# Performance work log

Hardware: AMD Instinct MI355X
Metric: run time of the kernel (lower is better)

## Reference

```python
import jax, jax.numpy as jnp
import numpy as np

N, E, F, T = 10000, 160000, 4, 12   # nodes, edges, features, periods
C, HID, OUT = 512, 256, 12          # tgcn out_channels, head hidden, output_dim


def setup_inputs() -> dict:
    key = jax.random.key(0)
    ks = jax.random.split(key, 24)
    g = lambda k, s: (jax.random.normal(k, s, dtype=jnp.float32) * 0.05)
    inp = {
        "x": jax.random.normal(ks[0], (N, F, T), dtype=jnp.float32),
        "edge_index": jax.random.randint(ks[1], (2, E), 0, N, dtype=jnp.int32),
        "edge_attr": jax.random.uniform(ks[2], (E,), dtype=jnp.float32),
        "att": g(ks[3], (T,)),
        # TGCN gates: GCNConv (W [F,C], b [C]) + Linear on cat([conv, H]) ([2C,C], [C])
        "Wz_g": g(ks[4], (F, C)), "bz_g": jnp.zeros((C,), jnp.float32),
        "Wz_l": g(ks[5], (2 * C, C)), "bz_l": jnp.zeros((C,), jnp.float32),
        "Wr_g": g(ks[6], (F, C)), "br_g": jnp.zeros((C,), jnp.float32),
        "Wr_l": g(ks[7], (2 * C, C)), "br_l": jnp.zeros((C,), jnp.float32),
        "Wh_g": g(ks[8], (F, C)), "bh_g": jnp.zeros((C,), jnp.float32),
        "Wh_l": g(ks[9], (2 * C, C)), "bh_l": jnp.zeros((C,), jnp.float32),
        # dense head
        "W1": g(ks[10], (C, HID)), "b1": jnp.zeros((HID,), jnp.float32),
        "W2": g(ks[11], (HID, OUT)), "b2": jnp.zeros((OUT,), jnp.float32),
    }
    return inp


def reference(x, edge_index, edge_attr, att,
              Wz_g, bz_g, Wz_l, bz_l,
              Wr_g, br_g, Wr_l, br_l,
              Wh_g, bh_g, Wh_l, bh_l,
              W1, b1, W2, b2):
    n = x.shape[0]
    # GCN normalization with self loops (fill value 1.0), computed once
    loops = jnp.arange(n, dtype=edge_index.dtype)
    src = jnp.concatenate([edge_index[0], loops])
    dst = jnp.concatenate([edge_index[1], loops])
    w = jnp.concatenate([edge_attr, jnp.ones((n,), x.dtype)])
    deg = jax.ops.segment_sum(w, dst, num_segments=n)
    dinv = jax.lax.rsqrt(jnp.maximum(deg, 1e-12))
    norm = dinv[src] * w * dinv[dst]  # [E+N]

    def gcn(xt, W, b):
        xw = xt @ W                                   # [N,C]
        msg = norm[:, None] * xw[src]                 # gather over edges
        return jax.ops.segment_sum(msg, dst, num_segments=n) + b

    probs = jax.nn.softmax(att)            # attention over periods
    xt_seq = jnp.moveaxis(x, -1, 0)        # [T,N,F]
    H0 = jnp.zeros((n, C), x.dtype)

    def step(carry, inp):
        H, acc = carry
        xt, p = inp
        z = jax.nn.sigmoid(jnp.concatenate([gcn(xt, Wz_g, bz_g), H], axis=1) @ Wz_l + bz_l)
        r = jax.nn.sigmoid(jnp.concatenate([gcn(xt, Wr_g, br_g), H], axis=1) @ Wr_l + br_l)
        ht = jnp.tanh(jnp.concatenate([gcn(xt, Wh_g, bh_g), H * r], axis=1) @ Wh_l + bh_l)
        Hn = z * H + (1.0 - z) * ht
        return (Hn, acc + p * Hn), None

    (Hf, H_accum), _ = jax.lax.scan(step, (H0, H0), (xt_seq, probs))
    out_hidden = H_accum
    h = jax.nn.relu(H_accum)
    h = jax.nn.relu(h @ W1 + b1)
    h = h @ W2 + b2
    return (h, out_hidden)
```

## Files before the change

### kernel.cpp

```cpp
#include <hip/hip_runtime.h>
#include <math.h>

#define NF 48
#define TT 12

typedef __bf16 v8bf __attribute__((ext_vector_type(8)));
typedef float v16f __attribute__((ext_vector_type(16)));

__device__ __forceinline__ void gld16(const void* g, void* l) {
  __builtin_amdgcn_global_load_lds(
      (const __attribute__((address_space(1))) void*)(uintptr_t)g,
      (__attribute__((address_space(3))) void*)(uintptr_t)l, 16, 0, 0);
}


__global__ void k_init(float* __restrict__ deg, int* __restrict__ cnt, int n) {
  int i = blockIdx.x * blockDim.x + threadIdx.x;
  if (i < n) { deg[i] = 1.0f; cnt[i] = 0; cnt[n + i] = 0; }
}

__global__ void k_edge(const int* __restrict__ dst, const float* __restrict__ w,
                       float* __restrict__ deg, int* __restrict__ cnt, int e) {
  int i = blockIdx.x * blockDim.x + threadIdx.x;
  if (i < e) {
    int d = dst[i];
    atomicAdd(&deg[d], w[i]);
    atomicAdd(&cnt[d], 1);
  }
}


__global__ void k_scan1(const int* __restrict__ cnt, int* __restrict__ pscan,
                        int* __restrict__ bsum, const float* __restrict__ deg,
                        float* __restrict__ dinv, int n) {
  __shared__ int s[256];
  int i = blockIdx.x * 256 + threadIdx.x;
  int v = (i < n) ? cnt[i] : 0;
  s[threadIdx.x] = v;
  __syncthreads();
  for (int off = 1; off < 256; off <<= 1) {
    int t = 0;
    if (threadIdx.x >= off) t = s[threadIdx.x - off];
    __syncthreads();
    s[threadIdx.x] += t;
    __syncthreads();
  }
  if (i < n) {
    pscan[i] = s[threadIdx.x] - v;
    dinv[i] = rsqrtf(fmaxf(deg[i], 1e-12f));
  }
  if (threadIdx.x == 255) bsum[blockIdx.x] = s[255];
}

__global__ void k_scan2(const int* __restrict__ bsum, int* __restrict__ bpre, int nb,
                        const float* __restrict__ att, float* __restrict__ probs) {
  if (blockIdx.x == 0 && threadIdx.x == 0) {
    int run = 0;
    for (int b = 0; b < nb; b++) { bpre[b] = run; run += bsum[b]; }
  }
  if (blockIdx.x == 0 && threadIdx.x == 64) {
    float m = -1e30f;
    for (int t = 0; t < TT; t++) m = fmaxf(m, att[t]);
    float e[TT], s = 0.f;
    for (int t = 0; t < TT; t++) { e[t] = expf(att[t] - m); s += e[t]; }
    for (int t = 0; t < TT; t++) probs[t] = e[t] / s;
  }
}

__global__ void k_scan3(const int* __restrict__ pscan, const int* __restrict__ bpre,
                        int* __restrict__ offs, int n, int e) {
  int i = blockIdx.x * blockDim.x + threadIdx.x;
  if (i < n) offs[i] = pscan[i] + bpre[i >> 8];
  if (i == 0) offs[n] = e;
}

__global__ void k_place(const int* __restrict__ src, const int* __restrict__ dst,
                        const float* __restrict__ w, const int* __restrict__ offs,
                        int* __restrict__ fill, int* __restrict__ csrc,
                        float* __restrict__ cw, int e) {
  int i = blockIdx.x * blockDim.x + threadIdx.x;
  if (i >= e) return;
  int d = dst[i];
  int p = offs[d] + atomicAdd(&fill[d], 1);
  csrc[p] = src[i];
  cw[p] = w[i];
}

__global__ void k_gather(const int* __restrict__ offs, const int* __restrict__ csrc,
                         const float* __restrict__ cw, const float* __restrict__ dinv,
                         const float* __restrict__ x, float* __restrict__ Y, int n) {
  int tg = blockIdx.x * blockDim.x + threadIdx.x;
  if (tg >= n * 12) return;
  int i = tg / 12, q = tg % 12;
  float di = dinv[i];
  const float4* x4 = (const float4*)x;
  float4 sv = x4[(size_t)i * 12 + q];
  float ax = di * sv.x, ay = di * sv.y, az = di * sv.z, aw = di * sv.w;
  int e1 = offs[i + 1];
  for (int e = offs[i]; e < e1; e++) {
    int s = csrc[e];
    float wv = cw[e] * dinv[s];
    float4 xv = x4[(size_t)s * 12 + q];
    ax = fmaf(wv, xv.x, ax); ay = fmaf(wv, xv.y, ay);
    az = fmaf(wv, xv.z, az); aw = fmaf(wv, xv.w, aw);
  }
  float4 o = make_float4(di * ax, di * ay, di * az, di * aw);
  ((float4*)Y)[(size_t)i * 12 + q] = o;
}

__device__ __forceinline__ size_t packIdx128(int n, int k) {
  int row = n & 127;
  int c = (k & 31) >> 3;
  return (size_t)(n >> 7) * (128 * 512) + (size_t)(k >> 5) * (128 * 32) +
         (size_t)row * 32 + (size_t)((c ^ (row & 3)) << 3) + (k & 7);
}

__global__ void k_pack3(const float* __restrict__ Wzl, const float* __restrict__ Wrl,
                        const float* __restrict__ Whl, const float* __restrict__ W1,
                        __bf16* __restrict__ WzrP, __bf16* __restrict__ WhP,
                        __bf16* __restrict__ W1P) {
  __shared__ __bf16 t[64][72];
  int modew = blockIdx.z;
  if (modew == 1 && blockIdx.x >= 8) return;
  if (modew == 2 && blockIdx.x >= 4) return;
  int n0 = blockIdx.x * 64, k0 = blockIdx.y * 64;
  __bf16* WT = (modew == 0) ? WzrP : (modew == 1) ? WhP : W1P;
#pragma unroll
  for (int p = 0; p < 4; p++) {
    int kk = p * 16 + (threadIdx.x >> 4);
    int nn = (threadIdx.x & 15) * 4;
    int n = n0 + nn, k = k0 + kk;
    float4 v;
    if (modew == 2) {
      v = *(const float4*)(W1 + (size_t)k * 256 + n);
    } else {
      const float* src = (modew == 1) ? Whl : Wzl;
      int nc = n;
      if (modew == 0 && n >= 512) { src = Wrl; nc = n - 512; }
      v = *(const float4*)(src + (size_t)(512 + k) * 512 + nc);
    }
    t[kk][nn + 0] = (__bf16)v.x; t[kk][nn + 1] = (__bf16)v.y;
    t[kk][nn + 2] = (__bf16)v.z; t[kk][nn + 3] = (__bf16)v.w;
  }
  __syncthreads();
#pragma unroll
  for (int u = 0; u < 2; u++) {
    int unit = threadIdx.x * 2 + u;
    int nl = unit >> 3, kg = unit & 7;
    v8bf o;
#pragma unroll
    for (int j = 0; j < 8; j++) o[j] = t[kg * 8 + j][nl];
    *(v8bf*)(WT + packIdx128(n0 + nl, k0 + kg * 8)) = o;
  }
}

__global__ void k_build_eff3(const float* __restrict__ Wzg, const float* __restrict__ Wzl,
                             const float* __restrict__ bzg, const float* __restrict__ bzl,
                             const float* __restrict__ Wrg, const float* __restrict__ Wrl,
                             const float* __restrict__ brg, const float* __restrict__ brl,
                             const float* __restrict__ Whg, const float* __restrict__ Whl,
                             const float* __restrict__ bhg, const float* __restrict__ bhl,
                             float* __restrict__ WzrE, float* __restrict__ bzrE,
                             float* __restrict__ WhE, float* __restrict__ bhE) {
  int idx = blockIdx.x * blockDim.x + threadIdx.x;
  if (idx >= 3 * 5 * 512) return;
  int seg = idx / 2560;
  int r = (idx % 2560) / 512, c = idx % 512;
  const float *Wg, *Wl, *bg, *bl;
  float *We, *be;
  int ostride, ooff;
  if (seg == 0) { Wg = Wzg; Wl = Wzl; bg = bzg; bl = bzl; We = WzrE; be = bzrE; ostride = 1024; ooff = 0; }
  else if (seg == 1) { Wg = Wrg; Wl = Wrl; bg = brg; bl = brl; We = WzrE; be = bzrE; ostride = 1024; ooff = 512; }
  else { Wg = Whg; Wl = Whl; bg = bhg; bl = bhl; We = WhE; be = bhE; ostride = 512; ooff = 0; }
  float s = 0.f;
  if (r < 4) {
    for (int k = 0; k < 512; k++) s += Wg[r * 512 + k] * Wl[k * 512 + c];
    We[r * ostride + ooff + c] = s;
  } else {
    for (int k = 0; k < 512; k++) s += bg[k] * Wl[k * 512 + c];
    be[ooff + c] = s + bl[c];
  }
}

__global__ void k_wy3(const float* __restrict__ WzrE, const float* __restrict__ bzrE,
                      const float* __restrict__ WhE, const float* __restrict__ bhE,
                      const float* __restrict__ b1,
                      __bf16* __restrict__ WyZR, __bf16* __restrict__ WyH,
                      __bf16* __restrict__ Wy1) {
  int idx = blockIdx.x * blockDim.x + threadIdx.x;
  const float* Weff; const float* beff; __bf16* out; int Nout, loc;
  if (idx < 1024 * 16) { Weff = WzrE; beff = bzrE; out = WyZR; Nout = 1024; loc = idx; }
  else if (idx < (1024 + 512) * 16) { Weff = WhE; beff = bhE; out = WyH; Nout = 512; loc = idx - 1024 * 16; }
  else if (idx < (1024 + 512 + 256) * 16) { Weff = nullptr; beff = b1; out = Wy1; Nout = 256; loc = idx - (1024 + 512) * 16; }
  else return;
  int n = loc >> 4, k = loc & 15;
  float v = 0.f;
  if (k < 4) v = Weff ? Weff[k * Nout + n] : 0.f;
  else if (k == 4) v = beff[n];
  out[(size_t)(n >> 7) * 2048 + (size_t)(n & 127) * 16 + k] = (__bf16)v;
}

__global__ void k_yat0(const float* __restrict__ Y,
                       const float* __restrict__ WzrE, const float* __restrict__ bzrE,
                       const float* __restrict__ WhE, const float* __restrict__ bhE,
                       __bf16* __restrict__ Ya, __bf16* __restrict__ H1, int n) {
  int idx = blockIdx.x * blockDim.x + threadIdx.x;
  int nt0 = n * 512;
  if (idx < nt0) {
    int i = idx >> 9, c = idx & 511;
    float y0 = Y[(size_t)i * NF + 0], y1 = Y[(size_t)i * NF + 12];
    float y2 = Y[(size_t)i * NF + 24], y3 = Y[(size_t)i * NF + 36];
    float pz = bzrE[c] + y0 * WzrE[c] + y1 * WzrE[1024 + c] +
               y2 * WzrE[2048 + c] + y3 * WzrE[3072 + c];
    float ph = bhE[c] + y0 * WhE[c] + y1 * WhE[512 + c] +
               y2 * WhE[1024 + c] + y3 * WhE[1536 + c];
    float z = 1.f / (1.f + expf(-pz));
    H1[idx] = (__bf16)((1.f - z) * tanhf(ph));
  } else {
    int r = idx - nt0;
    if (r >= TT * n * 16) return;
    int t = r / (n * 16);
    int loc = r % (n * 16);
    int nn = loc >> 4, k = loc & 15;
    float v = 0.f;
    if (k < 4) v = Y[(size_t)nn * NF + k * TT + t];
    else if (k == 4) v = 1.f;
    Ya[r] = (__bf16)v;
  }
}

template <int MODE>
__global__ __launch_bounds__(256, 6) void k_mm(
    const __bf16* __restrict__ Agm, const __bf16* __restrict__ Bp,
    const __bf16* __restrict__ Hc, const __bf16* __restrict__ Zbf,
    const __bf16* __restrict__ Ay, const __bf16* __restrict__ Wy,
    float* __restrict__ Ofp, __bf16* __restrict__ Obf, __bf16* __restrict__ ObfR,
    int M, int RB) {
  constexpr int CB = (MODE == 0) ? 8 : (MODE == 1) ? 4 : 2;
  constexpr int BUFS = 6144;
  __shared__ __bf16 smem[12288];

  int s = blockIdx.x;
  int grp = 8 * CB;
  int local = s % grp;
  int rowblk = (s / grp) * 8 + (local & 7);
  int colblk = local >> 3;
  if (rowblk >= RB) return;
  const int row0 = rowblk * 64;

  const int tid = threadIdx.x;
  const int lane = tid & 63, w = tid >> 6;
  const int wr = (w >> 1) * 32, wc = (w & 1) * 64;
  const int l31 = lane & 31, lh = lane >> 5;

  const int ar = tid >> 2, ac = tid & 3;
  const __bf16* At = Agm + (size_t)(row0 + ar) * 512 + ((ac ^ (ar & 3)) << 3);
  const __bf16* Bt = Bp + (size_t)colblk * (128 * 512);

  v16f acc[2];
#pragma unroll
  for (int j = 0; j < 2; j++)
#pragma unroll
    for (int q = 0; q < 16; q++) acc[j][q] = 0.f;

  auto stage = [&](int buf, int kt) {
    __bf16* base = smem + buf * BUFS;
    gld16(At + kt * 32, base + w * 512);
    const __bf16* bs = Bt + (size_t)kt * 4096 + (size_t)tid * 8;
    gld16(bs, base + 2048 + w * 512);
    gld16(bs + 2048, base + 4096 + w * 512);
  };
  auto stageY = [&](int buf) {
    __bf16* base = smem + buf * BUFS;
    if (w < 2)
      gld16(Ay + (size_t)(row0 + (tid >> 1)) * 16 + (tid & 1) * 8, base + w * 512);
    gld16(Wy + (size_t)colblk * 2048 + (size_t)tid * 8, base + 2048 + w * 512);
  };
  auto compute = [&](int buf) {
    const __bf16* base = smem + buf * BUFS;
#pragma unroll
    for (int ks = 0; ks < 2; ks++) {
      int kc = ks * 2 + lh;
      int fr = wr + l31;
      v8bf a = *(const v8bf*)&base[fr * 32 + ((kc ^ (fr & 3)) << 3)];
#pragma unroll
      for (int ni = 0; ni < 2; ni++) {
        int fc = wc + ni * 32 + l31;
        v8bf b = *(const v8bf*)&base[2048 + fc * 32 + ((kc ^ (fc & 3)) << 3)];
        acc[ni] = __builtin_amdgcn_mfma_f32_32x32x16_bf16(a, b, acc[ni], 0, 0, 0);
      }
    }
  };
  auto computeY = [&](int buf) {
    const __bf16* base = smem + buf * BUFS;
    v8bf a = *(const v8bf*)&base[(wr + l31) * 16 + lh * 8];
#pragma unroll
    for (int ni = 0; ni < 2; ni++) {
      v8bf b = *(const v8bf*)&base[2048 + (wc + ni * 32 + l31) * 16 + lh * 8];
      acc[ni] = __builtin_amdgcn_mfma_f32_32x32x16_bf16(a, b, acc[ni], 0, 0, 0);
    }
  };

  stage(0, 0);
  __syncthreads();
#pragma unroll
  for (int kt = 0; kt < 16; kt++) {
    int cur = kt & 1;
    if (kt < 15) stage(cur ^ 1, kt + 1);
    else stageY(cur ^ 1);
    compute(cur);
    __syncthreads();
  }
  computeY(0);
  __syncthreads();

  if constexpr (MODE == 2) {
#pragma unroll
    for (int ni = 0; ni < 2; ni++) {
      int cl = wc + ni * 32 + l31;
#pragma unroll
      for (int reg = 0; reg < 16; reg++) {
        int rg = row0 + wr + (reg & 3) + ((reg >> 2) << 3) + (lh << 2);
        if (rg >= M) continue;
        Ofp[(size_t)rg * 256 + colblk * 128 + cl] = fmaxf(acc[ni][reg], 0.f);
      }
    }
  } else if constexpr (MODE == 0) {
#pragma unroll
    for (int ni = 0; ni < 2; ni++) {
      int cl = wc + ni * 32 + l31;
#pragma unroll
      for (int reg = 0; reg < 16; reg++) {
        int lr = wr + (reg & 3) + ((reg >> 2) << 3) + (lh << 2);
        smem[lr * 128 + cl] = (__bf16)(1.f / (1.f + expf(-acc[ni][reg])));
      }
    }
    __syncthreads();
    int row = tid >> 2, seg = (tid & 3) * 32;
    int rg = row0 + row;
    if (rg < M) {
      int cof = (colblk & 3) * 128;
      if (colblk < 4) {
#pragma unroll
        for (int q = 0; q < 4; q++) {
          uint4 v = *(const uint4*)&smem[row * 128 + seg + q * 8];
          *(uint4*)(Obf + (size_t)rg * 512 + cof + seg + q * 8) = v;
        }
      } else {
#pragma unroll
        for (int q = 0; q < 4; q++) {
          v8bf r8 = *(const v8bf*)&smem[row * 128 + seg + q * 8];
          v8bf h8 = *(const v8bf*)(Agm + (size_t)rg * 512 + cof + seg + q * 8);
          v8bf o;
#pragma unroll
          for (int j = 0; j < 8; j++) o[j] = (__bf16)((float)r8[j] * (float)h8[j]);
          *(v8bf*)(ObfR + (size_t)rg * 512 + cof + seg + q * 8) = o;
        }
      }
    }
  } else {
    float* sF = (float*)smem;
#pragma unroll
    for (int h = 0; h < 2; h++) {
      if ((w >> 1) == h) {
#pragma unroll
        for (int ni = 0; ni < 2; ni++) {
          int cl = wc + ni * 32 + l31;
#pragma unroll
          for (int reg = 0; reg < 16; reg++) {
            int lr = (reg & 3) + ((reg >> 2) << 3) + (lh << 2);
            sF[lr * 128 + cl] = tanhf(acc[ni][reg]);
          }
        }
      }
      __syncthreads();
      int row = tid >> 3, seg = (tid & 7) * 16;
      int rg = row0 + h * 32 + row;
      if (rg < M) {
        int cg0 = colblk * 128 + seg;
#pragma unroll
        for (int q = 0; q < 2; q++) {
          v8bf z8 = *(const v8bf*)(Zbf + (size_t)rg * 512 + cg0 + q * 8);
          v8bf h8 = *(const v8bf*)(Hc + (size_t)rg * 512 + cg0 + q * 8);
          v8bf o;
#pragma unroll
          for (int j = 0; j < 8; j++) {
            float z = (float)z8[j];
            float ht = sF[row * 128 + seg + q * 8 + j];
            o[j] = (__bf16)(z * (float)h8[j] + (1.f - z) * ht);
          }
          *(v8bf*)(Obf + (size_t)rg * 512 + cg0 + q * 8) = o;
        }
      }
      if (h == 0) __syncthreads();
    }
  }
}

__global__ void k_acc(const __bf16* __restrict__ hist, const float* __restrict__ probs,
                      float* __restrict__ acc, __bf16* __restrict__ accRelu, int n) {
  int idx = blockIdx.x * blockDim.x + threadIdx.x;
  if (idx >= n * 64) return;
  size_t off = (size_t)idx * 8;
  size_t S = (size_t)n * 512;
  float s[8] = {0, 0, 0, 0, 0, 0, 0, 0};
#pragma unroll
  for (int t = 0; t < TT; t++) {
    float p = probs[t];
    v8bf h = *(const v8bf*)(hist + (size_t)(t + 1) * S + off);
#pragma unroll
    for (int j = 0; j < 8; j++) s[j] = fmaf(p, (float)h[j], s[j]);
  }
  *(float4*)(acc + off) = make_float4(s[0], s[1], s[2], s[3]);
  *(float4*)(acc + off + 4) = make_float4(s[4], s[5], s[6], s[7]);
  v8bf rl;
#pragma unroll
  for (int j = 0; j < 8; j++) rl[j] = (__bf16)fmaxf(s[j], 0.f);
  *(v8bf*)(accRelu + off) = rl;
}

__global__ void k_head2(const float* __restrict__ T1, const float* __restrict__ W2,
                        const float* __restrict__ b2, float* __restrict__ out0, int M) {
  int idx = blockIdx.x * blockDim.x + threadIdx.x;
  if (idx >= M * 12) return;
  int i = idx / 12, c = idx % 12;
  const float* tr = T1 + (size_t)i * 256;
  float s = b2[c];
  for (int k = 0; k < 256; k++) s = fmaf(tr[k], W2[k * 12 + c], s);
  out0[idx] = s;
}


extern "C" void kernel_launch(void* const* d_in, const int* in_sizes, int n_in,
                              void* d_out, int out_size, void* d_ws, size_t ws_size,
                              hipStream_t stream) {
  const float* x   = (const float*)d_in[0];
  const int*   ei  = (const int*)d_in[1];
  const float* ea  = (const float*)d_in[2];
  const float* att = (const float*)d_in[3];
  const float* Wzg = (const float*)d_in[4];  const float* bzg = (const float*)d_in[5];
  const float* Wzl = (const float*)d_in[6];  const float* bzl = (const float*)d_in[7];
  const float* Wrg = (const float*)d_in[8];  const float* brg = (const float*)d_in[9];
  const float* Wrl = (const float*)d_in[10]; const float* brl = (const float*)d_in[11];
  const float* Whg = (const float*)d_in[12]; const float* bhg = (const float*)d_in[13];
  const float* Whl = (const float*)d_in[14]; const float* bhl = (const float*)d_in[15];
  const float* W1  = (const float*)d_in[16]; const float* b1  = (const float*)d_in[17];
  const float* W2  = (const float*)d_in[18]; const float* b2  = (const float*)d_in[19];

  const int N = in_sizes[0] / NF;
  const int E = in_sizes[1] / 2;
  const int* srcI = ei;
  const int* dstI = ei + E;

  float* out0 = (float*)d_out;
  float* accO = (float*)d_out + (size_t)N * 12;

  char* wp = (char*)d_ws;
  auto carve = [&](size_t bytes) -> void* {
    void* p = (void*)wp;
    wp += (bytes + 255) & ~(size_t)255;
    return p;
  };
  float*  deg     = (float*)carve((size_t)N * 4);
  float*  dinv    = (float*)carve((size_t)N * 4);
  float*  probs   = (float*)carve(64);
  float*  Y       = (float*)carve((size_t)N * NF * 4);
  __bf16* WzrP    = (__bf16*)carve((size_t)1024 * 512 * 2);
  __bf16* WhP     = (__bf16*)carve((size_t)512 * 512 * 2);
  __bf16* W1P     = (__bf16*)carve((size_t)256 * 512 * 2);
  float*  Wzr_eff = (float*)carve((size_t)4 * 1024 * 4);
  float*  bzr_eff = (float*)carve((size_t)1024 * 4);
  float*  Wh_eff  = (float*)carve((size_t)4 * 512 * 4);
  float*  bh_eff  = (float*)carve((size_t)512 * 4);
  __bf16* hist    = (__bf16*)carve((size_t)(TT + 1) * N * 512 * 2);
  __bf16* Zbf     = (__bf16*)carve((size_t)N * 512 * 2);
  __bf16* Rbf     = (__bf16*)carve((size_t)N * 512 * 2);
  __bf16* accRelu = (__bf16*)carve((size_t)N * 512 * 2);
  float*  T1      = (float*)carve((size_t)N * 256 * 4);
  __bf16* Ya      = (__bf16*)carve((size_t)TT * N * 16 * 2);
  __bf16* WyZR    = (__bf16*)carve((size_t)1024 * 16 * 2);
  __bf16* WyH     = (__bf16*)carve((size_t)512 * 16 * 2);
  __bf16* Wy1     = (__bf16*)carve((size_t)256 * 16 * 2);
  int*    cnt     = (int*)carve((size_t)2 * N * 4);
  int*    fill    = cnt + N;
  int*    offs    = (int*)carve((size_t)(N + 1) * 4);
  int*    pscan   = (int*)carve((size_t)N * 4);
  int*    bsum    = (int*)carve(256);
  int*    bpre    = (int*)carve(256);
  int*    csrc    = (int*)carve((size_t)E * 4);
  float*  cw      = (float*)carve((size_t)E * 4);
  (void)carve(512 * 1024);
  (void)ws_size; (void)n_in; (void)out_size;

  const int TPB = 256;
  auto cdiv = [](int a, int b) { return (a + b - 1) / b; };
  const size_t S = (size_t)N * 512;

  k_init<<<cdiv(N, TPB), TPB, 0, stream>>>(deg, cnt, N);
  k_edge<<<cdiv(E, TPB), TPB, 0, stream>>>(dstI, ea, deg, cnt, E);

  const int nb = cdiv(N, 256);
  k_scan1<<<nb, 256, 0, stream>>>(cnt, pscan, bsum, deg, dinv, N);
  k_scan2<<<1, 128, 0, stream>>>(bsum, bpre, nb, att, probs);
  k_scan3<<<cdiv(N, TPB), TPB, 0, stream>>>(pscan, bpre, offs, N, E);
  k_place<<<cdiv(E, TPB), TPB, 0, stream>>>(srcI, dstI, ea, offs, fill, csrc, cw, E);
  k_gather<<<cdiv(N * 12, TPB), TPB, 0, stream>>>(offs, csrc, cw, dinv, x, Y, N);

  {
    dim3 gp(16, 8, 3);
    k_pack3<<<gp, 256, 0, stream>>>(Wzl, Wrl, Whl, W1, WzrP, WhP, W1P);
  }
  k_build_eff3<<<cdiv(3 * 5 * 512, TPB), TPB, 0, stream>>>(
      Wzg, Wzl, bzg, bzl, Wrg, Wrl, brg, brl, Whg, Whl, bhg, bhl,
      Wzr_eff, bzr_eff, Wh_eff, bh_eff);
  k_wy3<<<cdiv((1024 + 512 + 256) * 16, TPB), TPB, 0, stream>>>(
      Wzr_eff, bzr_eff, Wh_eff, bh_eff, b1, WyZR, WyH, Wy1);

  k_yat0<<<cdiv(N * 512 + TT * N * 16, TPB), TPB, 0, stream>>>(
      Y, Wzr_eff, bzr_eff, Wh_eff, bh_eff, Ya, hist + S, N);

  const int RB = cdiv(N, 64);
  const int nGrp = cdiv(RB, 8);
  for (int t = 1; t < TT; t++) {
    const __bf16* Hbt = hist + (size_t)t * S;
    __bf16* Hbn = hist + (size_t)(t + 1) * S;
    const __bf16* Yat = Ya + (size_t)t * N * 16;
    k_mm<0><<<64 * nGrp, 256, 0, stream>>>(Hbt, WzrP, nullptr, nullptr, Yat, WyZR,
                                           nullptr, Zbf, Rbf, N, RB);
    k_mm<1><<<32 * nGrp, 256, 0, stream>>>(Rbf, WhP, Hbt, Zbf, Yat, WyH,
                                           nullptr, Hbn, nullptr, N, RB);
  }

  k_acc<<<cdiv(N * 64, TPB), TPB, 0, stream>>>(hist, probs, accO, accRelu, N);
  k_mm<2><<<16 * nGrp, 256, 0, stream>>>(accRelu, W1P, nullptr, nullptr, Ya, Wy1,
                                         T1, nullptr, nullptr, N, RB);
  k_head2<<<cdiv(N * 12, TPB), TPB, 0, stream>>>(T1, W2, b2, out0, N);
}
```

Before: 709.8 us.

## Triple-buffer GEMM LDS pipeline, remap blocks per XCD, change LDS swizzle

Moves the GRU-step GEMM kernel from double buffering to a three-stage LDS pipeline. It issues two stages ahead and uses explicit vmcnt waits so global-to-LDS loads overlap more compute. The small Y-augmentation tile is loaded up front into its own LDS region. Blocks are remapped so each XCD owns a contiguous range of row blocks, which should improve L2 reuse of A tiles across column blocks. The LDS XOR swizzle now keys on row>>1 to cut bank conflicts, MFMA sections raise wave priority, and occupancy drops to 4 waves per SIMD because of the larger LDS footprint.

New measurement: 673.0 us. -5.2%, faster.

```diff
diff --git a/kernel.cpp b/kernel.cpp
--- a/kernel.cpp
+++ b/kernel.cpp
@@ -112,7 +112,7 @@
   int row = n & 127;
   int c = (k & 31) >> 3;
   return (size_t)(n >> 7) * (128 * 512) + (size_t)(k >> 5) * (128 * 32) +
-         (size_t)row * 32 + (size_t)((c ^ (row & 3)) << 3) + (k & 7);
+         (size_t)row * 32 + (size_t)((c ^ ((row >> 1) & 3)) << 3) + (k & 7);
 }
 
 __global__ void k_pack3(const float* __restrict__ Wzl, const float* __restrict__ Wrl,
@@ -230,169 +230,175 @@
 }
 
 template <int MODE>
-__global__ __launch_bounds__(256, 6) void k_mm(
+__global__ __launch_bounds__(256, 4) void k_mm(
     const __bf16* __restrict__ Agm, const __bf16* __restrict__ Bp,
     const __bf16* __restrict__ Hc, const __bf16* __restrict__ Zbf,
     const __bf16* __restrict__ Ay, const __bf16* __restrict__ Wy,
     float* __restrict__ Ofp, __bf16* __restrict__ Obf, __bf16* __restrict__ ObfR,
     int M, int RB) {
-  constexpr int CB = (MODE == 0) ? 8 : (MODE == 1) ? 4 : 2;
   constexpr int BUFS = 6144;
-  __shared__ __bf16 smem[12288];
-
-  int s = blockIdx.x;
-  int grp = 8 * CB;
-  int local = s % grp;
-  int rowblk = (s / grp) * 8 + (local & 7);
-  int colblk = local >> 3;
-  if (rowblk >= RB) return;
-  const int row0 = rowblk * 64;
-
-  const int tid = threadIdx.x;
-  const int lane = tid & 63, w = tid >> 6;
-  const int wr = (w >> 1) * 32, wc = (w & 1) * 64;
-  const int l31 = lane & 31, lh = lane >> 5;
-
-  const int ar = tid >> 2, ac = tid & 3;
-  const __bf16* At = Agm + (size_t)(row0 + ar) * 512 + ((ac ^ (ar & 3)) << 3);
-  const __bf16* Bt = Bp + (size_t)colblk * (128 * 512);
-
-  v16f acc[2];
-#pragma unroll
-  for (int j = 0; j < 2; j++)
-#pragma unroll
-    for (int q = 0; q < 16; q++) acc[j][q] = 0.f;
-
-  auto stage = [&](int buf, int kt) {
-    __bf16* base = smem + buf * BUFS;
-    gld16(At + kt * 32, base + w * 512);
-    const __bf16* bs = Bt + (size_t)kt * 4096 + (size_t)tid * 8;
-    gld16(bs, base + 2048 + w * 512);
-    gld16(bs + 2048, base + 4096 + w * 512);
-  };
-  auto stageY = [&](int buf) {
-    __bf16* base = smem + buf * BUFS;
-    if (w < 2)
-      gld16(Ay + (size_t)(row0 + (tid >> 1)) * 16 + (tid & 1) * 8, base + w * 512);
-    gld16(Wy + (size_t)colblk * 2048 + (size_t)tid * 8, base + 2048 + w * 512);
-  };
-  auto compute = [&](int buf) {
-    const __bf16* base = smem + buf * BUFS;
-#pragma unroll
-    for (int ks = 0; ks < 2; ks++) {
-      int kc = ks * 2 + lh;
-      int fr = wr + l31;
-      v8bf a = *(const v8bf*)&base[fr * 32 + ((kc ^ (fr & 3)) << 3)];
+  __shared__ __bf16 smem[21504];
+
+  const int RBX = (RB + 7) >> 3;
+  {
+    int xcd = blockIdx.x & 7;
+    int idx = blockIdx.x >> 3;
+    int rowblk = xcd * RBX + idx % RBX;
+    int colblk = idx / RBX;
+    if (rowblk >= RB) return;
+
+    const int row0 = rowblk * 64;
+    const int tid = threadIdx.x;
+    const int lane = tid & 63, w = tid >> 6;
+    const int wr = (w >> 1) * 32, wc = (w & 1) * 64;
+    const int l31 = lane & 31, lh = lane >> 5;
+
+    const int ar = tid >> 2, ac = tid & 3;
+    const __bf16* At = Agm + (size_t)(row0 + ar) * 512 + ((ac ^ ((ar >> 1) & 3)) << 3);
+    const __bf16* Bt = Bp + (size_t)colblk * (128 * 512);
+
+    v16f acc[2];
+#pragma unroll
+    for (int j = 0; j < 2; j++)
+#pragma unroll
+      for (int q = 0; q < 16; q++) acc[j][q] = 0.f;
+
+    auto stage = [&](int buf, int kt) {
+      __bf16* base = smem + buf * BUFS;
+      gld16(At + kt * 32, base + w * 512);
+      const __bf16* bs = Bt + (size_t)kt * 4096 + (size_t)tid * 8;
+      gld16(bs, base + 2048 + w * 512);
+      gld16(bs + 2048, base + 4096 + w * 512);
+    };
+    auto stageY = [&]() {
+      if (w < 2)
+        gld16(Ay + (size_t)(row0 + (tid >> 1)) * 16 + (tid & 1) * 8,
+              smem + 18432 + w * 512);
+      gld16(Wy + (size_t)colblk * 2048 + (size_t)tid * 8, smem + 19456 + w * 512);
+    };
+    auto compute = [&](int buf) {
+      const __bf16* base = smem + buf * BUFS;
+      __builtin_amdgcn_s_setprio(1);
+#pragma unroll
+      for (int ks = 0; ks < 2; ks++) {
+        int kc = ks * 2 + lh;
+        int fr = wr + l31;
+        v8bf a = *(const v8bf*)&base[fr * 32 + ((kc ^ ((fr >> 1) & 3)) << 3)];
+#pragma unroll
+        for (int ni = 0; ni < 2; ni++) {
+          int fc = wc + ni * 32 + l31;
+          v8bf b = *(const v8bf*)&base[2048 + fc * 32 + ((kc ^ ((fc >> 1) & 3)) << 3)];
+          acc[ni] = __builtin_amdgcn_mfma_f32_32x32x16_bf16(a, b, acc[ni], 0, 0, 0);
+        }
+      }
+      __builtin_amdgcn_s_setprio(0);
+    };
+    auto computeY = [&]() {
+      const __bf16* ya = smem + 18432;
+      const __bf16* yb = smem + 19456;
+      v8bf a = *(const v8bf*)&ya[(wr + l31) * 16 + lh * 8];
 #pragma unroll
       for (int ni = 0; ni < 2; ni++) {
-        int fc = wc + ni * 32 + l31;
-        v8bf b = *(const v8bf*)&base[2048 + fc * 32 + ((kc ^ (fc & 3)) << 3)];
+        v8bf b = *(const v8bf*)&yb[(wc + ni * 32 + l31) * 16 + lh * 8];
         acc[ni] = __builtin_amdgcn_mfma_f32_32x32x16_bf16(a, b, acc[ni], 0, 0, 0);
       }
+    };
+
+    stageY();
+    stage(0, 0);
+    stage(1, 1);
+#pragma unroll
+    for (int kt = 0; kt < 16; kt++) {
+      if (kt < 15)
+        asm volatile("s_waitcnt vmcnt(3) lgkmcnt(0)\n\ts_barrier" ::: "memory");
+      else
+        asm volatile("s_waitcnt vmcnt(0) lgkmcnt(0)\n\ts_barrier" ::: "memory");
+      if (kt < 14) stage((kt + 2) % 3, kt + 2);
+      compute(kt % 3);
     }
-  };
-  auto computeY = [&](int buf) {
-    const __bf16* base = smem + buf * BUFS;
-    v8bf a = *(const v8bf*)&base[(wr + l31) * 16 + lh * 8];
-#pragma unroll
-    for (int ni = 0; ni < 2; ni++) {
-      v8bf b = *(const v8bf*)&base[2048 + (wc + ni * 32 + l31) * 16 + lh * 8];
-      acc[ni] = __builtin_amdgcn_mfma_f32_32x32x16_bf16(a, b, acc[ni], 0, 0, 0);
-    }
-  };
-
-  stage(0, 0);
-  __syncthreads();
-#pragma unroll
-  for (int kt = 0; kt < 16; kt++) {
-    int cur = kt & 1;
-    if (kt < 15) stage(cur ^ 1, kt + 1);
-    else stageY(cur ^ 1);
-    compute(cur);
+    computeY();
     __syncthreads();
-  }
-  computeY(0);
-  __syncthreads();
-
-  if constexpr (MODE == 2) {
-#pragma unroll
-    for (int ni = 0; ni < 2; ni++) {
-      int cl = wc + ni * 32 + l31;
-#pragma unroll
-      for (int reg = 0; reg < 16; reg++) {
-        int rg = row0 + wr + (reg & 3) + ((reg >> 2) << 3) + (lh << 2);
-        if (rg >= M) continue;
-        Ofp[(size_t)rg * 256 + colblk * 128 + cl] = fmaxf(acc[ni][reg], 0.f);
-      }
-    }
-  } else if constexpr (MODE == 0) {
-#pragma unroll
-    for (int ni = 0; ni < 2; ni++) {
-      int cl = wc + ni * 32 + l31;
-#pragma unroll
-      for (int reg = 0; reg < 16; reg++) {
-        int lr = wr + (reg & 3) + ((reg >> 2) << 3) + (lh << 2);
-        smem[lr * 128 + cl] = (__bf16)(1.f / (1.f + expf(-acc[ni][reg])));
-      }
-    }
-    __syncthreads();
-    int row = tid >> 2, seg = (tid & 3) * 32;
-    int rg = row0 + row;
-    if (rg < M) {
-      int cof = (colblk & 3) * 128;
-      if (colblk < 4) {
-#pragma unroll
-        for (int q = 0; q < 4; q++) {
-          uint4 v = *(const uint4*)&smem[row * 128 + seg + q * 8];
-          *(uint4*)(Obf + (size_t)rg * 512 + cof + seg + q * 8) = v;
-        }
-      } else {
-#pragma unroll
-        for (int q = 0; q < 4; q++) {
-          v8bf r8 = *(const v8bf*)&smem[row * 128 + seg + q * 8];
-          v8bf h8 = *(const v8bf*)(Agm + (size_t)rg * 512 + cof + seg + q * 8);
-          v8bf o;
-#pragma unroll
-          for (int j = 0; j < 8; j++) o[j] = (__bf16)((float)r8[j] * (float)h8[j]);
-          *(v8bf*)(ObfR + (size_t)rg * 512 + cof + seg + q * 8) = o;
+
+    if constexpr (MODE == 2) {
+#pragma unroll
+      for (int ni = 0; ni < 2; ni++) {
+        int cl = wc + ni * 32 + l31;
+#pragma unroll
+        for (int reg = 0; reg < 16; reg++) {
+          int rg = row0 + wr + (reg & 3) + ((reg >> 2) << 3) + (lh << 2);
+          if (rg >= M) continue;
+          Ofp[(size_t)rg * 256 + colblk * 128 + cl] = fmaxf(acc[ni][reg], 0.f);
         }
       }
-    }
-  } else {
-    float* sF = (float*)smem;
-#pragma unroll
-    for (int h = 0; h < 2; h++) {
-      if ((w >> 1) == h) {
-#pragma unroll
-        for (int ni = 0; ni < 2; ni++) {
-          int cl = wc + ni * 32 + l31;
-#pragma unroll
-          for (int reg = 0; reg < 16; reg++) {
-            int lr = (reg & 3) + ((reg >> 2) << 3) + (lh << 2);
-            sF[lr * 128 + cl] = tanhf(acc[ni][reg]);
+    } else if constexpr (MODE == 0) {
+#pragma unroll
+      for (int ni = 0; ni < 2; ni++) {
+        int cl = wc + ni * 32 + l31;
+#pragma unroll
+        for (int reg = 0; reg < 16; reg++) {
+          int lr = wr + (reg & 3) + ((reg >> 2) << 3) + (lh << 2);
+          smem[lr * 128 + cl] = (__bf16)(1.f / (1.f + expf(-acc[ni][reg])));
+        }
+      }
+      __syncthreads();
+      int row = tid >> 2, seg = (tid & 3) * 32;
+      int rg = row0 + row;
+      if (rg < M) {
+        int cof = (colblk & 3) * 128;
+        if (colblk < 4) {
+#pragma unroll
+          for (int q = 0; q < 4; q++) {
+            uint4 v = *(const uint4*)&smem[row * 128 + seg + q * 8];
+            *(uint4*)(Obf + (size_t)rg * 512 + cof + seg + q * 8) = v;
+          }
+        } else {
+#pragma unroll
+          for (int q = 0; q < 4; q++) {
+            v8bf r8 = *(const v8bf*)&smem[row * 128 + seg + q * 8];
+            v8bf h8 = *(const v8bf*)(Agm + (size_t)rg * 512 + cof + seg + q * 8);
+            v8bf o;
+#pragma unroll
+            for (int j = 0; j < 8; j++) o[j] = (__bf16)((float)r8[j] * (float)h8[j]);
+            *(v8bf*)(ObfR + (size_t)rg * 512 + cof + seg + q * 8) = o;
           }
         }
       }
-      __syncthreads();
-      int row = tid >> 3, seg = (tid & 7) * 16;
-      int rg = row0 + h * 32 + row;
-      if (rg < M) {
-        int cg0 = colblk * 128 + seg;
-#pragma unroll
-        for (int q = 0; q < 2; q++) {
-          v8bf z8 = *(const v8bf*)(Zbf + (size_t)rg * 512 + cg0 + q * 8);
-          v8bf h8 = *(const v8bf*)(Hc + (size_t)rg * 512 + cg0 + q * 8);
-          v8bf o;
-#pragma unroll
-          for (int j = 0; j < 8; j++) {
-            float z = (float)z8[j];
-            float ht = sF[row * 128 + seg + q * 8 + j];
-            o[j] = (__bf16)(z * (float)h8[j] + (1.f - z) * ht);
+    } else {
+      float* sF = (float*)smem;
+#pragma unroll
+      for (int h = 0; h < 2; h++) {
+        if ((w >> 1) == h) {
+#pragma unroll
+          for (int ni = 0; ni < 2; ni++) {
+            int cl = wc + ni * 32 + l31;
+#pragma unroll
+            for (int reg = 0; reg < 16; reg++) {
+              int lr = (reg & 3) + ((reg >> 2) << 3) + (lh << 2);
+              sF[lr * 128 + cl] = tanhf(acc[ni][reg]);
+            }
           }
-          *(v8bf*)(Obf + (size_t)rg * 512 + cg0 + q * 8) = o;
         }
+        __syncthreads();
+        int row = tid >> 3, seg = (tid & 7) * 16;
+        int rg = row0 + h * 32 + row;
+        if (rg < M) {
+          int cg0 = colblk * 128 + seg;
+#pragma unroll
+          for (int q = 0; q < 2; q++) {
+            v8bf z8 = *(const v8bf*)(Zbf + (size_t)rg * 512 + cg0 + q * 8);
+            v8bf h8 = *(const v8bf*)(Hc + (size_t)rg * 512 + cg0 + q * 8);
+            v8bf o;
+#pragma unroll
+            for (int j = 0; j < 8; j++) {
+              float z = (float)z8[j];
+              float ht = sF[row * 128 + seg + q * 8 + j];
+              o[j] = (__bf16)(z * (float)h8[j] + (1.f - z) * ht);
+            }
+            *(v8bf*)(Obf + (size_t)rg * 512 + cg0 + q * 8) = o;
+          }
+        }
+        if (h == 0) __syncthreads();
       }
-      if (h == 0) __syncthreads();
     }
   }
 }
@@ -479,7 +485,7 @@
   float*  T1      = (float*)carve((size_t)N * 256 * 4);
   __bf16* Ya      = (__bf16*)carve((size_t)TT * N * 16 * 2);
   __bf16* WyZR    = (__bf16*)carve((size_t)1024 * 16 * 2);
-  __bf16* WyH     = (__bf16*)carve((size_t)512 * 16 * 2);
+  __bf16* WyH    = (__bf16*)carve((size_t)512 * 16 * 2);
   __bf16* Wy1     = (__bf16*)carve((size_t)256 * 16 * 2);
   int*    cnt     = (int*)carve((size_t)2 * N * 4);
   int*    fill    = cnt + N;
@@ -520,19 +526,19 @@
       Y, Wzr_eff, bzr_eff, Wh_eff, bh_eff, Ya, hist + S, N);
 
   const int RB = cdiv(N, 64);
-  const int nGrp = cdiv(RB, 8);
+  const int RBX = cdiv(RB, 8);
   for (int t = 1; t < TT; t++) {
     const __bf16* Hbt = hist + (size_t)t * S;
     __bf16* Hbn = hist + (size_t)(t + 1) * S;
     const __bf16* Yat = Ya + (size_t)t * N * 16;
-    k_mm<0><<<64 * nGrp, 256, 0, stream>>>(Hbt, WzrP, nullptr, nullptr, Yat, WyZR,
-                                           nullptr, Zbf, Rbf, N, RB);
-    k_mm<1><<<32 * nGrp, 256, 0, stream>>>(Rbf, WhP, Hbt, Zbf, Yat, WyH,
-                                           nullptr, Hbn, nullptr, N, RB);
+    k_mm<0><<<8 * RBX * 8, 256, 0, stream>>>(Hbt, WzrP, nullptr, nullptr, Yat, WyZR,
+                                             nullptr, Zbf, Rbf, N, RB);
+    k_mm<1><<<8 * RBX * 4, 256, 0, stream>>>(Rbf, WhP, Hbt, Zbf, Yat, WyH,
+                                             nullptr, Hbn, nullptr, N, RB);
   }
 
   k_acc<<<cdiv(N * 64, TPB), TPB, 0, stream>>>(hist, probs, accO, accRelu, N);
-  k_mm<2><<<16 * nGrp, 256, 0, stream>>>(accRelu, W1P, nullptr, nullptr, Ya, Wy1,
-                                         T1, nullptr, nullptr, N, RB);
+  k_mm<2><<<8 * RBX * 2, 256, 0, stream>>>(accRelu, W1P, nullptr, nullptr, Ya, Wy1,
+                                           T1, nullptr, nullptr, N, RB);
   k_head2<<<cdiv(N * 12, TPB), TPB, 0, stream>>>(T1, W2, b2, out0, N);
 }
```
